# Kernel tuning notes

Hardware: AMD Instinct MI355X
Metric: run time of the kernel (lower is better)

## Reference

```python
import jax, jax.numpy as jnp
import numpy as np

WS = (7, 7, 7)          # window size (s, h, w)
N_TOK = WS[0] * WS[1] * WS[2]   # 343
DIM = 96
HEADS = 3
N_WINDOWS = 64
BATCH = 8
B_ = BATCH * N_WINDOWS  # 512


def _rel_pos_index(ws):
    s, h, w = ws
    coords = np.stack(np.meshgrid(np.arange(s), np.arange(h), np.arange(w), indexing='ij'))
    cf = coords.reshape(3, -1)                     # [3, N]
    rel = cf[:, :, None] - cf[:, None, :]          # [3, N, N]
    rel = rel.transpose(1, 2, 0).astype(np.int64)  # [N, N, 3]
    rel[..., 0] += s - 1
    rel[..., 1] += h - 1
    rel[..., 2] += w - 1
    rel[..., 0] *= (2 * h - 1) * (2 * w - 1)
    rel[..., 1] *= (2 * w - 1)
    return rel.sum(-1)                             # [N, N] in [0, (2s-1)(2h-1)(2w-1))


def setup_inputs() -> dict:
    key = jax.random.key(0)
    ks = jax.random.split(key, 8)
    table_len = (2 * WS[0] - 1) * (2 * WS[1] - 1) * (2 * WS[2] - 1)  # 2197
    return {
        'x': jax.random.normal(ks[0], (B_, N_TOK, DIM), dtype=jnp.float32),
        'mask': jax.random.normal(ks[1], (N_WINDOWS, N_TOK, N_TOK), dtype=jnp.float32),
        'qkv_w': jax.random.normal(ks[2], (3 * DIM, DIM), dtype=jnp.float32) * 0.02,
        'qkv_b': jax.random.normal(ks[3], (3 * DIM,), dtype=jnp.float32) * 0.02,
        'proj_w': jax.random.normal(ks[4], (DIM, DIM), dtype=jnp.float32) * 0.02,
        'proj_b': jax.random.normal(ks[5], (DIM,), dtype=jnp.float32) * 0.02,
        'rpb_table': jax.random.normal(ks[6], (table_len, HEADS), dtype=jnp.float32) * 0.02,
        'rel_index': jnp.asarray(_rel_pos_index(WS), dtype=jnp.int32),
    }


def reference(x, mask, qkv_w, qkv_b, proj_w, proj_b, rpb_table, rel_index):
    B, N, C = x.shape
    H = rpb_table.shape[1]
    hd = C // H
    scale = hd ** -0.5

    qkv = x @ qkv_w.T + qkv_b                         # [B, N, 3C]
    qkv = qkv.reshape(B, N, 3, H, hd).transpose(2, 0, 3, 1, 4)  # [3, B, H, N, hd]
    q, k, v = qkv[0] * scale, qkv[1], qkv[2]

    attn = jnp.einsum('bhnd,bhmd->bhnm', q, k)        # [B, H, N, N]
    bias = rpb_table[rel_index].transpose(2, 0, 1)    # [H, N, N]
    attn = attn + bias[None]

    nW = mask.shape[0]
    attn = attn.reshape(B // nW, nW, H, N, N) + mask[None, :, None]
    attn = jax.nn.softmax(attn.reshape(B, H, N, N), axis=-1)

    out = jnp.einsum('bhnm,bhmd->bnhd', attn, v).reshape(B, N, C)
    return out @ proj_w.T + proj_b
```

## Files before the change

kernel.cpp:

```cpp
#include <hip/hip_runtime.h>
#include <stdint.h>

#define NTOK 343
#define L2E 1.4426950408889634f
#define SCALE (0.17677669529663687f * 1.4426950408889634f)

typedef uint32_t u32a __attribute__((may_alias));
typedef __attribute__((ext_vector_type(8))) short short8;
typedef short8 bfrag __attribute__((may_alias));
typedef __attribute__((ext_vector_type(4))) float f32x4;
typedef f32x4 f32x4a __attribute__((may_alias));
typedef __attribute__((ext_vector_type(2))) uint32_t u32x2;
typedef u32x2 u32x2a __attribute__((may_alias));

static __device__ __forceinline__ uint16_t f2bf(float f) {
    uint32_t u = __float_as_uint(f);
    u += 0x7fffu + ((u >> 16) & 1u);
    return (uint16_t)(u >> 16);
}
static __device__ __forceinline__ float bflo(uint32_t p) { return __uint_as_float(p << 16); }
static __device__ __forceinline__ float bfhi(uint32_t p) { return __uint_as_float(p & 0xffff0000u); }

static __device__ __forceinline__ float exp2_fast(float x) {
    float r;
    __asm__("v_exp_f32 %0, %1" : "=v"(r) : "v"(x));
    return r;
}
static __device__ __forceinline__ uint32_t cvtpk_bf16(float lo, float hi) {
    uint32_t r;
    __asm__("v_cvt_pk_bf16_f32 %0, %1, %2" : "=v"(r) : "v"(lo), "v"(hi));
    return r;
}

union abits { uint32_t u[4]; bfrag f; };

__global__ __launch_bounds__(256) void comb_pre(const float* __restrict__ mask,
                                                const float* __restrict__ rpb,
                                                const int* __restrict__ rel,
                                                u32a* __restrict__ comb) {
    int e = blockIdx.x * 256 + threadIdx.x;
    const int total = 64 * NTOK * 176;
    if (e >= total) return;
    int m16 = e & 15;
    int tp = (e >> 4) % 11;
    int rest = e / 176;
    int i = rest % NTOK;
    int w = rest / NTOK;
    int j0 = tp * 32 + m16;
    int j1 = j0 + 16;
    const float* mrow = mask + ((size_t)w * NTOK + i) * NTOK;
    const int* rrow = rel + i * NTOK;
    float mk0 = mrow[j0];
    int r0 = rrow[j0] * 3;
    const bool ok1 = (j1 < NTOK);
    float mk1 = ok1 ? mrow[j1] : 0.f;
    int r1 = ok1 ? rrow[j1] * 3 : 0;
    u32a* cbase = comb + ((size_t)(w * 3) * NTOK + i) * 176 + tp * 16 + m16;
    #pragma unroll
    for (int h = 0; h < 3; ++h) {
        float c0 = (mk0 + rpb[r0 + h]) * L2E;
        uint32_t hi = 0xFF80u;
        if (ok1) hi = (uint32_t)f2bf((mk1 + rpb[r1 + h]) * L2E);
        cbase[(size_t)h * (NTOK * 176)] = (uint32_t)f2bf(c0) | (hi << 16);
    }
}

#define QKV_LOADX(DST, ROW) do { \
    const float* xr_ = x + (size_t)(ROW) * 96 + quad * 8; \
    DST##0 = *(const f32x4a*)(xr_); \
    DST##1 = *(const f32x4a*)(xr_ + 4); \
    DST##2 = *(const f32x4a*)(xr_ + 32); \
    DST##3 = *(const f32x4a*)(xr_ + 36); \
    DST##4 = *(const f32x4a*)(xr_ + 64); \
    DST##5 = *(const f32x4a*)(xr_ + 68); \
} while (0)

#define QKV_COMPUTE(SRC, ITC) do { \
    abits A0_, A1_, A2_; \
    A0_.u[0] = cvtpk_bf16(SRC##0[0], SRC##0[1]); \
    A0_.u[1] = cvtpk_bf16(SRC##0[2], SRC##0[3]); \
    A0_.u[2] = cvtpk_bf16(SRC##1[0], SRC##1[1]); \
    A0_.u[3] = cvtpk_bf16(SRC##1[2], SRC##1[3]); \
    A1_.u[0] = cvtpk_bf16(SRC##2[0], SRC##2[1]); \
    A1_.u[1] = cvtpk_bf16(SRC##2[2], SRC##2[3]); \
    A1_.u[2] = cvtpk_bf16(SRC##3[0], SRC##3[1]); \
    A1_.u[3] = cvtpk_bf16(SRC##3[2], SRC##3[3]); \
    A2_.u[0] = cvtpk_bf16(SRC##4[0], SRC##4[1]); \
    A2_.u[1] = cvtpk_bf16(SRC##4[2], SRC##4[3]); \
    A2_.u[2] = cvtpk_bf16(SRC##5[0], SRC##5[1]); \
    A2_.u[3] = cvtpk_bf16(SRC##5[2], SRC##5[3]); \
    const int rowc = row0 + (ITC) * 16; \
    const int bbc = rowc / 343; \
    const int nnc = rowc - bbc * 343; \
    _Pragma("unroll") \
    for (int ct = 0; ct < 18; ++ct) { \
        f32x4 Cl = (f32x4){0.f, 0.f, 0.f, 0.f}; \
        bfrag w0_ = *(const bfrag*)(w_l + (ct * 16 + m) * 104 + quad * 8); \
        Cl = __builtin_amdgcn_mfma_f32_16x16x32_bf16(w0_, A0_.f, Cl, 0, 0, 0); \
        bfrag w1_ = *(const bfrag*)(w_l + (ct * 16 + m) * 104 + 32 + quad * 8); \
        Cl = __builtin_amdgcn_mfma_f32_16x16x32_bf16(w1_, A1_.f, Cl, 0, 0, 0); \
        bfrag w2_ = *(const bfrag*)(w_l + (ct * 16 + m) * 104 + 64 + quad * 8); \
        Cl = __builtin_amdgcn_mfma_f32_16x16x32_bf16(w2_, A2_.f, Cl, 0, 0, 0); \
        f32x4 b4_ = *(const f32x4*)(bias_l + ct * 16 + 4 * quad); \
        f32x4 vv_ = Cl + b4_; \
        const int sel_ = ct / 6; \
        const int base_ = (ct % 6) * 16 + 4 * quad; \
        const int hd_ = base_ >> 5, dd_ = base_ & 31; \
        uint32_t lo_ = cvtpk_bf16(vv_[0], vv_[1]); \
        uint32_t hi_ = cvtpk_bf16(vv_[2], vv_[3]); \
        u32x2 pk_ = {lo_, hi_}; \
        *(u32x2a*)(dsts[sel_] + ((size_t)(bbc * 3 + hd_) * NTOK + nnc) * 32 + dd_) = pk_; \
    } \
} while (0)

__global__ __launch_bounds__(512, 4) void qkv_kernel(
    const float* __restrict__ x, const float* __restrict__ qkv_w,
    const float* __restrict__ qkv_b,
    uint16_t* __restrict__ q_ws, uint16_t* __restrict__ k_ws, uint16_t* __restrict__ v_ws)
{
    __shared__ uint16_t w_l[288 * 104];
    __shared__ __align__(16) float bias_l[288];
    const int tid = threadIdx.x;

    {
        f32x4 tmp[14];
        #pragma unroll
        for (int i = 0; i < 14; ++i) {
            int idx = tid + i * 512;
            if (idx < 6912) tmp[i] = ((const f32x4a*)qkv_w)[idx];
        }
        for (int e = tid; e < 288; e += 512) {
            float bb = qkv_b[e];
            bias_l[e] = (e < 96) ? bb * SCALE : bb;
        }
        #pragma unroll
        for (int i = 0; i < 14; ++i) {
            int idx = tid + i * 512;
            if (idx < 6912) {
                int c = idx / 24, k = (idx - c * 24) * 4;
                f32x4 v = tmp[i];
                float s = (c < 96) ? SCALE : 1.f;
                uint32_t lo = cvtpk_bf16(v[0] * s, v[1] * s);
                uint32_t hi = cvtpk_bf16(v[2] * s, v[3] * s);
                u32x2 pk = {lo, hi};
                *(u32x2a*)(w_l + c * 104 + k) = pk;
            }
        }
    }
    __syncthreads();

    const int lane = tid & 63, wv8 = tid >> 6;
    const int m = lane & 15, quad = lane >> 4;

    uint16_t* const dsts[3] = {q_ws, k_ws, v_ws};
    const int row0 = blockIdx.x * 256 + wv8 * 32 + m;

    f32x4 tA0, tA1, tA2, tA3, tA4, tA5;
    f32x4 tB0, tB1, tB2, tB3, tB4, tB5;
    QKV_LOADX(tA, row0);
    QKV_LOADX(tB, row0 + 16);
    QKV_COMPUTE(tA, 0);
    QKV_COMPUTE(tB, 1);
}

__global__ __launch_bounds__(256, 2) void attn_kernel(
    uint16_t* __restrict__ q_ws, const uint16_t* __restrict__ k_ws,
    const uint16_t* __restrict__ v_ws, const u32a* __restrict__ comb)
{
    __shared__ uint16_t k_l[352 * 40];
    __shared__ uint16_t vT[32 * 360];
    __shared__ uint16_t pstage[4][16 * 104];

    const int bh = blockIdx.x;
    const int b = bh / 3, h = bh - b * 3, w = b & 63;
    const int tid = threadIdx.x, lane = tid & 63, wv = tid >> 6;
    const int m = lane & 15, quad = lane >> 4;
    const int wh = w * 3 + h;

    const u32a* ksrc = (const u32a*)(k_ws + (size_t)bh * NTOK * 32);
    const u32a* vsrc = (const u32a*)(v_ws + (size_t)bh * NTOK * 32);
    u32a* k32 = (u32a*)k_l;
    {
        uint32_t tk[22], tv[22];
        #pragma unroll
        for (int i = 0; i < 22; ++i) {
            int e = tid + i * 256;
            if (e < NTOK * 16) { tk[i] = ksrc[e]; tv[i] = vsrc[e]; }
        }
        #pragma unroll
        for (int i = 0; i < 22; ++i) {
            int e = tid + i * 256;
            if (e < NTOK * 16) {
                int tok = e >> 4, dp = e & 15;
                k32[tok * 20 + dp] = tk[i];
                uint32_t vv = tv[i];
                int kp = ((tok >> 5) << 5) + ((tok & 15) << 1) + ((tok >> 4) & 1);
                vT[(2 * dp) * 360 + kp]     = (uint16_t)(vv & 0xffffu);
                vT[(2 * dp + 1) * 360 + kp] = (uint16_t)(vv >> 16);
            }
        }
    }
    for (int e = tid; e < 9 * 16; e += 256) {
        int tok = 343 + (e >> 4), dp = e & 15;
        k32[tok * 20 + dp] = 0;
    }
    for (int e = tid; e < 32 * 9; e += 256) {
        int d = e / 9, tok = 343 + (e % 9);
        int kp = ((tok >> 5) << 5) + ((tok & 15) << 1) + ((tok >> 4) & 1);
        vT[d * 360 + kp] = 0;
    }
    __syncthreads();

    uint16_t* qbase = q_ws + (size_t)bh * NTOK * 32;
    uint16_t* stg = pstage[wv];

    for (int ti = wv; ti < 22; ti += 4) {
        const int i0 = ti * 16;
        bfrag qf = *(const bfrag*)(qbase + (size_t)(i0 + m) * 32 + quad * 8);
        uint32_t cw[4][11];
        #pragma unroll
        for (int r = 0; r < 4; ++r) {
            int ir = i0 + 4 * quad + r;
            ir = (ir > 342) ? 342 : ir;
            const u32a* crow = comb + ((size_t)(wh * NTOK + ir)) * 176 + m;
            #pragma unroll
            for (int tp = 0; tp < 11; ++tp)
                cw[r][tp] = crow[tp * 16];
        }

        f32x4 S[22];
        #pragma unroll
        for (int t = 0; t < 22; ++t) S[t] = (f32x4){0.f, 0.f, 0.f, 0.f};
        __builtin_amdgcn_s_setprio(1);
        #pragma unroll
        for (int t = 0; t < 22; ++t) {
            bfrag kf = *(const bfrag*)(k_l + (t * 16 + m) * 40 + quad * 8);
            S[t] = __builtin_amdgcn_mfma_f32_16x16x32_bf16(qf, kf, S[t], 0, 0, 0);
        }
        __builtin_amdgcn_s_setprio(0);

        float sum[4] = {0.f, 0.f, 0.f, 0.f};

        f32x4 O0 = (f32x4){0.f, 0.f, 0.f, 0.f};
        f32x4 O1 = (f32x4){0.f, 0.f, 0.f, 0.f};
        #pragma unroll
        for (int qt = 0; qt < 4; ++qt) {
            const int nch = (qt == 3) ? 2 : 3;
            #pragma unroll
            for (int uu = 0; uu < 3; ++uu) {
                if (uu < nch) {
                    const int tp = qt * 3 + uu;
                    #pragma unroll
                    for (int r = 0; r < 4; ++r) {
                        float e0 = exp2_fast(S[2 * tp][r] + bflo(cw[r][tp]));
                        float e1 = exp2_fast(S[2 * tp + 1][r] + bfhi(cw[r][tp]));
                        sum[r] += e0 + e1;
                        *(u32a*)(stg + (4 * quad + r) * 104 + uu * 32 + 2 * m) =
                            cvtpk_bf16(e0, e1);
                    }
                }
            }
            __asm__ __volatile__("" ::: "memory");
            __builtin_amdgcn_s_waitcnt(0xC07F);
            __asm__ __volatile__("" ::: "memory");

            __builtin_amdgcn_s_setprio(1);
            #pragma unroll
            for (int c = 0; c < 3; ++c) {
                if (c < nch) {
                    const int jj = qt * 96 + c * 32;
                    bfrag pf = *(const bfrag*)(stg + m * 104 + c * 32 + quad * 8);
                    bfrag v0 = *(const bfrag*)(vT + (size_t)m * 360 + jj + quad * 8);
                    bfrag v1 = *(const bfrag*)(vT + (size_t)(m + 16) * 360 + jj + quad * 8);
                    O0 = __builtin_amdgcn_mfma_f32_16x16x32_bf16(pf, v0, O0, 0, 0, 0);
                    O1 = __builtin_amdgcn_mfma_f32_16x16x32_bf16(pf, v1, O1, 0, 0, 0);
                }
            }
            __builtin_amdgcn_s_setprio(0);
            __asm__ __volatile__("" ::: "memory");
        }

        float inv_[4];
        #pragma unroll
        for (int r = 0; r < 4; ++r) {
            float v = sum[r];
            v += __shfl_xor(v, 1);
            v += __shfl_xor(v, 2);
            v += __shfl_xor(v, 4);
            v += __shfl_xor(v, 8);
            inv_[r] = 1.f / v;
        }

        #pragma unroll
        for (int r = 0; r < 4; ++r) {
            const int ir = i0 + 4 * quad + r;
            if (ir < NTOK) {
                uint16_t* orow = qbase + (size_t)ir * 32;
                orow[m]      = f2bf(O0[r] * inv_[r]);
                orow[m + 16] = f2bf(O1[r] * inv_[r]);
            }
        }
    }
}

#define PROJ_LOADA(DST, RM) do { \
    const int bm_ = (RM) / 343; \
    const int nm_ = (RM) - bm_ * 343; \
    const uint16_t* ab_ = ao + ((size_t)(bm_ * 3) * NTOK + nm_) * 32 + quad * 8; \
    DST##0 = *(const bfrag*)(ab_); \
    DST##1 = *(const bfrag*)(ab_ + (size_t)NTOK * 32); \
    DST##2 = *(const bfrag*)(ab_ + (size_t)(2 * NTOK) * 32); \
} while (0)

#define PROJ_COMPUTE(SRC, ITC) do { \
    float* orow_ = out + (size_t)(row0 + (ITC) * 16) * 96 + 4 * quad; \
    _Pragma("unroll") \
    for (int ct = 0; ct < 6; ++ct) { \
        f32x4 Cl = (f32x4){0.f, 0.f, 0.f, 0.f}; \
        bfrag w0_ = *(const bfrag*)(w_l + (ct * 16 + m) * 104 + quad * 8); \
        Cl = __builtin_amdgcn_mfma_f32_16x16x32_bf16(w0_, SRC##0, Cl, 0, 0, 0); \
        bfrag w1_ = *(const bfrag*)(w_l + (ct * 16 + m) * 104 + 32 + quad * 8); \
        Cl = __builtin_amdgcn_mfma_f32_16x16x32_bf16(w1_, SRC##1, Cl, 0, 0, 0); \
        bfrag w2_ = *(const bfrag*)(w_l + (ct * 16 + m) * 104 + 64 + quad * 8); \
        Cl = __builtin_amdgcn_mfma_f32_16x16x32_bf16(w2_, SRC##2, Cl, 0, 0, 0); \
        *(f32x4a*)(orow_ + ct * 16) = Cl + bp4[ct]; \
    } \
} while (0)

__global__ __launch_bounds__(256) void proj_kernel(
    const uint16_t* __restrict__ ao, const float* __restrict__ proj_w,
    const float* __restrict__ proj_b, float* __restrict__ out)
{
    __shared__ uint16_t w_l[96 * 104];
    const int tid = threadIdx.x;
    {
        f32x4 tmp[9];
        #pragma unroll
        for (int i = 0; i < 9; ++i)
            tmp[i] = ((const f32x4a*)proj_w)[tid + i * 256];
        #pragma unroll
        for (int i = 0; i < 9; ++i) {
            int c4 = tid + i * 256;
            int c = c4 / 24, k = (c4 - c * 24) * 4;
            f32x4 v = tmp[i];
            uint32_t lo = cvtpk_bf16(v[0], v[1]);
            uint32_t hi = cvtpk_bf16(v[2], v[3]);
            u32x2 pk = {lo, hi};
            *(u32x2a*)(w_l + c * 104 + k) = pk;
        }
    }
    __syncthreads();

    const int lane = tid & 63, wv4 = tid >> 6;
    const int m = lane & 15, quad = lane >> 4;

    f32x4 bp4[6];
    #pragma unroll
    for (int ct = 0; ct < 6; ++ct)
        bp4[ct] = *(const f32x4a*)(proj_b + ct * 16 + 4 * quad);

    const int row0 = blockIdx.x * 256 + wv4 * 64 + m;

    bfrag aA0, aA1, aA2, aB0, aB1, aB2;
    PROJ_LOADA(aA, row0);
    PROJ_LOADA(aB, row0 + 16);
    PROJ_COMPUTE(aA, 0);
    PROJ_LOADA(aA, row0 + 32);
    PROJ_COMPUTE(aB, 1);
    PROJ_LOADA(aB, row0 + 48);
    PROJ_COMPUTE(aA, 2);
    PROJ_COMPUTE(aB, 3);
}

extern "C" void kernel_launch(void* const* d_in, const int* in_sizes, int n_in,
                              void* d_out, int out_size, void* d_ws, size_t ws_size,
                              hipStream_t stream) {
    const float* x      = (const float*)d_in[0];
    const float* mask   = (const float*)d_in[1];
    const float* qkv_w  = (const float*)d_in[2];
    const float* qkv_b  = (const float*)d_in[3];
    const float* proj_w = (const float*)d_in[4];
    const float* proj_b = (const float*)d_in[5];
    const float* rpb    = (const float*)d_in[6];
    const int*   rel    = (const int*)d_in[7];
    float* out = (float*)d_out;

    uint16_t* q_ws = (uint16_t*)d_ws;
    uint16_t* k_ws = q_ws + 16859136;
    uint16_t* v_ws = k_ws + 16859136;
    u32a* comb = (u32a*)((char*)d_ws + 101154816);

    const int comb_total = 64 * NTOK * 176;
    comb_pre<<<dim3((comb_total + 255) / 256), 256, 0, stream>>>(mask, rpb, rel, comb);
    qkv_kernel<<<dim3(686), 512, 0, stream>>>(x, qkv_w, qkv_b, q_ws, k_ws, v_ws);
    attn_kernel<<<dim3(512 * 3), 256, 0, stream>>>(q_ws, k_ws, v_ws, comb);
    proj_kernel<<<dim3(686), 256, 0, stream>>>(q_ws, proj_w, proj_b, out);
}
```

Baseline: 288.1 us.

## Compute softmax row sums via MFMA with ones, repad LDS, remap blocks for XCD locality

```diff
diff --git a/kernel.cpp b/kernel.cpp
--- a/kernel.cpp
+++ b/kernel.cpp
@@ -167,15 +167,23 @@
     uint16_t* __restrict__ q_ws, const uint16_t* __restrict__ k_ws,
     const uint16_t* __restrict__ v_ws, const u32a* __restrict__ comb)
 {
-    __shared__ uint16_t k_l[352 * 40];
-    __shared__ uint16_t vT[32 * 360];
-    __shared__ uint16_t pstage[4][16 * 104];
-
-    const int bh = blockIdx.x;
-    const int b = bh / 3, h = bh - b * 3, w = b & 63;
+    __shared__ uint16_t k_l[352 * 42];
+    __shared__ uint16_t vT[32 * 354];
+    __shared__ uint16_t pstage[4][16 * 102];
+
+    const int bid = blockIdx.x;
+    const int xcd = bid & 7;
+    const int j = bid >> 3;
+    const int w = xcd + 8 * (j & 7);
+    const int rest = j >> 3;
+    const int h = rest % 3;
+    const int bt = rest / 3;
+    const int b = bt * 64 + w;
+    const int bh = b * 3 + h;
+    const int wh = w * 3 + h;
+
     const int tid = threadIdx.x, lane = tid & 63, wv = tid >> 6;
     const int m = lane & 15, quad = lane >> 4;
-    const int wh = w * 3 + h;
 
     const u32a* ksrc = (const u32a*)(k_ws + (size_t)bh * NTOK * 32);
     const u32a* vsrc = (const u32a*)(v_ws + (size_t)bh * NTOK * 32);
@@ -192,27 +200,31 @@
             int e = tid + i * 256;
             if (e < NTOK * 16) {
                 int tok = e >> 4, dp = e & 15;
-                k32[tok * 20 + dp] = tk[i];
+                k32[tok * 21 + dp] = tk[i];
                 uint32_t vv = tv[i];
                 int kp = ((tok >> 5) << 5) + ((tok & 15) << 1) + ((tok >> 4) & 1);
-                vT[(2 * dp) * 360 + kp]     = (uint16_t)(vv & 0xffffu);
-                vT[(2 * dp + 1) * 360 + kp] = (uint16_t)(vv >> 16);
+                vT[(2 * dp) * 354 + kp]     = (uint16_t)(vv & 0xffffu);
+                vT[(2 * dp + 1) * 354 + kp] = (uint16_t)(vv >> 16);
             }
         }
     }
     for (int e = tid; e < 9 * 16; e += 256) {
         int tok = 343 + (e >> 4), dp = e & 15;
-        k32[tok * 20 + dp] = 0;
+        k32[tok * 21 + dp] = 0;
     }
     for (int e = tid; e < 32 * 9; e += 256) {
         int d = e / 9, tok = 343 + (e % 9);
         int kp = ((tok >> 5) << 5) + ((tok & 15) << 1) + ((tok >> 4) & 1);
-        vT[d * 360 + kp] = 0;
+        vT[d * 354 + kp] = 0;
     }
     __syncthreads();
 
     uint16_t* qbase = q_ws + (size_t)bh * NTOK * 32;
     uint16_t* stg = pstage[wv];
+
+    abits one_;
+    one_.u[0] = 0x3F803F80u; one_.u[1] = 0x3F803F80u;
+    one_.u[2] = 0x3F803F80u; one_.u[3] = 0x3F803F80u;
 
     for (int ti = wv; ti < 22; ti += 4) {
         const int i0 = ti * 16;
@@ -234,15 +246,14 @@
         __builtin_amdgcn_s_setprio(1);
         #pragma unroll
         for (int t = 0; t < 22; ++t) {
-            bfrag kf = *(const bfrag*)(k_l + (t * 16 + m) * 40 + quad * 8);
+            bfrag kf = *(const bfrag*)(k_l + (t * 16 + m) * 42 + quad * 8);
             S[t] = __builtin_amdgcn_mfma_f32_16x16x32_bf16(qf, kf, S[t], 0, 0, 0);
         }
         __builtin_amdgcn_s_setprio(0);
-
-        float sum[4] = {0.f, 0.f, 0.f, 0.f};
 
         f32x4 O0 = (f32x4){0.f, 0.f, 0.f, 0.f};
         f32x4 O1 = (f32x4){0.f, 0.f, 0.f, 0.f};
+        f32x4 Os = (f32x4){0.f, 0.f, 0.f, 0.f};
         #pragma unroll
         for (int qt = 0; qt < 4; ++qt) {
             const int nch = (qt == 3) ? 2 : 3;
@@ -254,8 +265,7 @@
                     for (int r = 0; r < 4; ++r) {
                         float e0 = exp2_fast(S[2 * tp][r] + bflo(cw[r][tp]));
                         float e1 = exp2_fast(S[2 * tp + 1][r] + bfhi(cw[r][tp]));
-                        sum[r] += e0 + e1;
-                        *(u32a*)(stg + (4 * quad + r) * 104 + uu * 32 + 2 * m) =
+                        *(u32a*)(stg + (4 * quad + r) * 102 + uu * 32 + 2 * m) =
                             cvtpk_bf16(e0, e1);
                     }
                 }
@@ -269,35 +279,26 @@
             for (int c = 0; c < 3; ++c) {
                 if (c < nch) {
                     const int jj = qt * 96 + c * 32;
-                    bfrag pf = *(const bfrag*)(stg + m * 104 + c * 32 + quad * 8);
-                    bfrag v0 = *(const bfrag*)(vT + (size_t)m * 360 + jj + quad * 8);
-                    bfrag v1 = *(const bfrag*)(vT + (size_t)(m + 16) * 360 + jj + quad * 8);
+                    bfrag pf = *(const bfrag*)(stg + m * 102 + c * 32 + quad * 8);
+                    bfrag v0 = *(const bfrag*)(vT + (size_t)m * 354 + jj + quad * 8);
+                    bfrag v1 = *(const bfrag*)(vT + (size_t)(m + 16) * 354 + jj + quad * 8);
                     O0 = __builtin_amdgcn_mfma_f32_16x16x32_bf16(pf, v0, O0, 0, 0, 0);
                     O1 = __builtin_amdgcn_mfma_f32_16x16x32_bf16(pf, v1, O1, 0, 0, 0);
+                    Os = __builtin_amdgcn_mfma_f32_16x16x32_bf16(pf, one_.f, Os, 0, 0, 0);
                 }
             }
             __builtin_amdgcn_s_setprio(0);
             __asm__ __volatile__("" ::: "memory");
-        }
-
-        float inv_[4];
-        #pragma unroll
-        for (int r = 0; r < 4; ++r) {
-            float v = sum[r];
-            v += __shfl_xor(v, 1);
-            v += __shfl_xor(v, 2);
-            v += __shfl_xor(v, 4);
-            v += __shfl_xor(v, 8);
-            inv_[r] = 1.f / v;
         }
 
         #pragma unroll
         for (int r = 0; r < 4; ++r) {
             const int ir = i0 + 4 * quad + r;
             if (ir < NTOK) {
+                const float inv_ = 1.f / Os[r];
                 uint16_t* orow = qbase + (size_t)ir * 32;
-                orow[m]      = f2bf(O0[r] * inv_[r]);
-                orow[m + 16] = f2bf(O1[r] * inv_[r]);
+                orow[m]      = f2bf(O0[r] * inv_);
+                orow[m + 16] = f2bf(O1[r] * inv_);
             }
         }
     }
```

New measurement: 321.0 us. 11.4% more time.
